# Performance work log

Measured on AMD Instinct MI355X. Metric: run time of the kernel, lower is better.

## Reference

```python
import jax, jax.numpy as jnp
import numpy as np

H, W = 352, 1216
K = 8                 # points_per_pixel (z-buffer depth)
RADIUS_PX = 1.5       # splat radius in pixels
RAD_POW = 2.0         # opts.rad_pow
TAU = 1.0             # opts.tau


def _rasterize(pts):
    # pts: [B,P,3] with xy in NDC [-1,1], z>0.
    # Returns idx [B,H,W,K] int32 (packed point index, -1 = empty),
    # dist2 [B,H,W,K] squared NDC distance to pixel center, and NDC radius r.
    B, P, _ = pts.shape
    r = RADIUS_PX / max(H, W) * 2.0
    hx = int(np.ceil(r * W / 2.0))   # splat half-extent in pixels (x)
    hy = int(np.ceil(r * H / 2.0))   # splat half-extent in pixels (y)
    dy, dx = np.meshgrid(np.arange(-hy, hy + 1), np.arange(-hx, hx + 1), indexing='ij')
    dy = jnp.asarray(dy.ravel()); dx = jnp.asarray(dx.ravel())     # [Wn]
    x, y, z = pts[..., 0], pts[..., 1], pts[..., 2]                # [B,P]
    i0 = jnp.floor((y + 1.0) * 0.5 * H).astype(jnp.int32)
    j0 = jnp.floor((x + 1.0) * 0.5 * W).astype(jnp.int32)
    ii = i0[..., None] + dy                                        # [B,P,Wn]
    jj = j0[..., None] + dx
    xc = (jj + 0.5) * (2.0 / W) - 1.0                              # pixel centers (NDC)
    yc = (ii + 0.5) * (2.0 / H) - 1.0
    d2 = (x[..., None] - xc) ** 2 + (y[..., None] - yc) ** 2
    valid = (ii >= 0) & (ii < H) & (jj >= 0) & (jj < W) & (d2 < r * r) & (z[..., None] > 0)
    NPIX = B * H * W
    pix = jnp.where(valid, (jnp.arange(B)[:, None, None] * H + ii) * W + jj, NPIX)
    pid = jnp.broadcast_to((jnp.arange(B)[:, None] * P + jnp.arange(P)[None, :])[..., None], pix.shape)
    pixf = pix.reshape(-1)
    zf = jnp.broadcast_to(z[..., None], pix.shape).reshape(-1)
    d2f = d2.reshape(-1)
    pidf = pid.reshape(-1)
    # sort candidates by (pixel, z): gives nearest-first z-buffer ordering per pixel
    order = jnp.lexsort((zf, pixf))
    pixs, d2s, pids = pixf[order], d2f[order], pidf[order]
    first = jnp.searchsorted(pixs, pixs, side='left')
    rank = jnp.arange(pixs.shape[0]) - first      # z-rank within each pixel
    keep = (rank < K) & (pixs < NPIX)
    tp = jnp.where(keep, pixs, NPIX)              # sentinel row NPIX collects rejects
    tr = jnp.where(keep, rank, 0)
    idx = jnp.full((NPIX + 1, K), -1, jnp.int32).at[tp, tr].set(
        jnp.where(keep, pids, -1).astype(jnp.int32))
    dist2 = jnp.zeros((NPIX + 1, K), pts.dtype).at[tp, tr].set(
        jnp.where(keep, d2s, jnp.zeros((), pts.dtype)))
    return idx[:NPIX].reshape(B, H, W, K), dist2[:NPIX].reshape(B, H, W, K), r


def _forward(pts3D, src):
    B, C, P = src.shape
    idx, dist2, r = _rasterize(pts3D)
    dist = dist2 / (r ** RAD_POW)
    alphas = (1.0 - jnp.sqrt(jnp.clip(dist, 0.001, 1.0))) ** TAU   # [B,H,W,K]
    feats = src.transpose(0, 2, 1).reshape(B * P, C)               # features_packed [B*P,C]
    acc = jnp.zeros((B, H, W, C), src.dtype)
    for k in range(K):   # fixed small depth-layer loop: weighted_sum compositing
        ik = idx[..., k]
        wk = jnp.where(ik >= 0, alphas[..., k], 0.0)
        acc = acc + wk[..., None] * feats[jnp.clip(ik, 0)]
    return acc.transpose(0, 3, 1, 2)                               # [B,C,H,W]


def setup_inputs():
    key = jax.random.key(0)
    k1, k2, k3 = jax.random.split(key, 3)
    B, P, C = 2, 65536, 64
    xy = jax.random.uniform(k1, (B, P, 2), minval=-1.0, maxval=1.0)
    z = jax.random.uniform(k2, (B, P, 1), minval=0.5, maxval=20.0)
    pts3D = jnp.concatenate([xy, z], axis=-1)
    src = jax.random.normal(k3, (B, C, P), dtype=jnp.float32)
    return {"pts3D": pts3D, "src": src}


def reference(pts3D, src):
    return _forward(pts3D, src)
```

## Files before the change

kernel.cpp:

```cpp
#include <hip/hip_runtime.h>
#include <cstdint>
#include <cstddef>

#define HH 352
#define WW 1216
#define KK 8
#define PP 65536
#define BB 2
#define CC 64

#define RD (1.5 / 1216.0 * 2.0)


static __device__ __forceinline__ unsigned int bf16pack_rn(float a, float b) {
    unsigned int ua = __float_as_uint(a), ub = __float_as_uint(b);
    ua = (ua + 0x7FFFu + ((ua >> 16) & 1u)) >> 16;
    ub = (ub + 0x7FFFu + ((ub >> 16) & 1u)) >> 16;
    return (ub << 16) | ua;
}

static __device__ __forceinline__ void scatter_body(const float* __restrict__ pts,
                                                    unsigned int* __restrict__ slots,
                                                    int tid) {
    const int b = tid >> 16;
    const float x = pts[tid * 3 + 0];
    const float y = pts[tid * 3 + 1];
    const float z = pts[tid * 3 + 2];
    if (!(z > 0.f)) return;

    const int i0 = (int)floorf((y + 1.f) * 0.5f * (float)HH);
    if (i0 < 0 || i0 >= HH) return;
    const int j0 = (int)floorf((x + 1.f) * 0.5f * (float)WW);

    const float yc = ((float)i0 + 0.5f) * (2.f / (float)HH) - 1.f;
    const float dyv = y - yc;
    const float dy2 = dyv * dyv;
    const float r2 = (float)(RD * RD);

    unsigned int fb = __float_as_uint(z) >> 13;
    fb = fb < 0x1F800u ? 0x1F800u : fb;
    fb = fb > 0x217FFu ? 0x217FFu : fb;
    const unsigned int key = ((fb - 0x1F800u) << 17) | (unsigned int)tid;

    const unsigned int rowbase = (unsigned int)(b * HH + i0) * WW;

    #pragma unroll
    for (int dx = -1; dx <= 1; ++dx) {
        const int jj = j0 + dx;
        if (jj < 0 || jj >= WW) continue;
        const float xc = ((float)jj + 0.5f) * (2.f / (float)WW) - 1.f;
        const float dxv = x - xc;
        if (!(dxv * dxv + dy2 < r2)) continue;

        unsigned int* s = slots + (size_t)(rowbase + jj) * KK;
        unsigned int cur = key;
        #pragma unroll
        for (int k = 0; k < KK; ++k) {
            unsigned int old = atomicMin(&s[k], cur);
            if (old & 0x80000000u) break;
            cur = old > cur ? old : cur;
        }
    }
}

#define TRANS_BLOCKS (BB * (PP / 64))
#define SCATTER_BLOCKS ((BB * PP) / 256)

__global__ __launch_bounds__(256) void prep_kernel(const float* __restrict__ pts,
                                                   const float* __restrict__ src,
                                                   unsigned int* __restrict__ slots,
                                                   unsigned int* __restrict__ feats) {
    __shared__ float tile[64][65];
    if (blockIdx.x < TRANS_BLOCKS) {
        const int bid = blockIdx.x;
        const int b = bid >> 10;
        const int p0 = (bid & 1023) * 64;
        const float* sb = src + (size_t)b * CC * PP;
        #pragma unroll
        for (int i = 0; i < 16; ++i) {
            const int idx = threadIdx.x + i * 256;
            const int c = idx >> 6;
            const int p = idx & 63;
            tile[p][c] = sb[(size_t)c * PP + (p0 + p)];
        }
        __syncthreads();
        unsigned int* fbp = feats + ((size_t)b * PP + p0) * (CC / 2);
        #pragma unroll
        for (int i = 0; i < 8; ++i) {
            const int idx = threadIdx.x + i * 256;
            const int p = idx >> 5;
            const int cp = idx & 31;
            fbp[(size_t)p * (CC / 2) + cp] = bf16pack_rn(tile[p][2 * cp], tile[p][2 * cp + 1]);
        }
        return;
    }
    scatter_body(pts, slots, (blockIdx.x - TRANS_BLOCKS) * 256 + threadIdx.x);
}

__global__ __launch_bounds__(256) void scatter_kernel(const float* __restrict__ pts,
                                                      unsigned int* __restrict__ slots) {
    scatter_body(pts, slots, blockIdx.x * 256 + threadIdx.x);
}

__global__ __launch_bounds__(256) void composite_kernel(const float* __restrict__ pts,
                                                        const unsigned int* __restrict__ feats,
                                                        const unsigned int* __restrict__ slots,
                                                        float* __restrict__ out) {
    const int HWp = HH * WW;
    const int pix = blockIdx.x * 64 + (threadIdx.x & 63);
    const int cg  = threadIdx.x >> 6;
    const int b  = pix / HWp;
    const int hw = pix - b * HWp;
    const int h = hw / WW;
    const int w = hw - h * WW;

    const uint4* sv = (const uint4*)(slots + (size_t)pix * KK);
    const uint4 sa = sv[0], sb4 = sv[1];
    const unsigned int keys[KK] = {sa.x, sa.y, sa.z, sa.w, sb4.x, sb4.y, sb4.z, sb4.w};

    const float xc = ((float)w + 0.5f) * (2.f / (float)WW) - 1.f;
    const float yc = ((float)h + 0.5f) * (2.f / (float)HH) - 1.f;
    const float invr2 = (float)(1.0 / (RD * RD));

    float acc[16];
    #pragma unroll
    for (int c = 0; c < 16; ++c) acc[c] = 0.f;

    #pragma unroll
    for (int k = 0; k < KK; ++k) {
        const unsigned int key = keys[k];
        if (key & 0x80000000u) break;
        const int pid = (int)(key & 0x1FFFFu);
        const float px = pts[pid * 3 + 0];
        const float py = pts[pid * 3 + 1];
        const float ddx = px - xc;
        const float ddy = py - yc;
        float dist = (ddx * ddx + ddy * ddy) * invr2;
        dist = fminf(fmaxf(dist, 0.001f), 1.0f);
        const float a = 1.f - sqrtf(dist);

        const uint4* f = (const uint4*)(feats + (size_t)pid * (CC / 2) + cg * 8);
        #pragma unroll
        for (int j = 0; j < 2; ++j) {
            const uint4 q = f[j];
            acc[8 * j + 0] += a * __uint_as_float(q.x << 16);
            acc[8 * j + 1] += a * __uint_as_float(q.x & 0xFFFF0000u);
            acc[8 * j + 2] += a * __uint_as_float(q.y << 16);
            acc[8 * j + 3] += a * __uint_as_float(q.y & 0xFFFF0000u);
            acc[8 * j + 4] += a * __uint_as_float(q.z << 16);
            acc[8 * j + 5] += a * __uint_as_float(q.z & 0xFFFF0000u);
            acc[8 * j + 6] += a * __uint_as_float(q.w << 16);
            acc[8 * j + 7] += a * __uint_as_float(q.w & 0xFFFF0000u);
        }
    }

    float* ob = out + (size_t)b * CC * HWp + (size_t)(cg * 16) * HWp + hw;
    #pragma unroll
    for (int c = 0; c < 16; ++c)
        __builtin_nontemporal_store(acc[c], ob + (size_t)c * HWp);
}

__global__ __launch_bounds__(256) void composite_direct(const float* __restrict__ pts,
                                                        const float* __restrict__ src,
                                                        const unsigned int* __restrict__ slots,
                                                        float* __restrict__ out) {
    const int HWp = HH * WW;
    const int tid = blockIdx.x * blockDim.x + threadIdx.x;
    const int b = tid / HWp;
    const int hw = tid - b * HWp;
    const int h = hw / WW;
    const int w = hw - h * WW;

    const uint4* sv = (const uint4*)(slots + (size_t)tid * KK);
    const uint4 sa = sv[0], sb4 = sv[1];
    const unsigned int keys[KK] = {sa.x, sa.y, sa.z, sa.w, sb4.x, sb4.y, sb4.z, sb4.w};

    const float xc = ((float)w + 0.5f) * (2.f / (float)WW) - 1.f;
    const float yc = ((float)h + 0.5f) * (2.f / (float)HH) - 1.f;
    const float invr2 = (float)(1.0 / (RD * RD));

    float alpha[KK];
    int   pidx[KK];
    int n = 0;
    #pragma unroll
    for (int k = 0; k < KK; ++k) {
        const unsigned int key = keys[k];
        if (key & 0x80000000u) break;
        const int pid = (int)(key & 0x1FFFFu);
        const float px = pts[pid * 3 + 0];
        const float py = pts[pid * 3 + 1];
        const float ddx = px - xc;
        const float ddy = py - yc;
        float dist = (ddx * ddx + ddy * ddy) * invr2;
        dist = fminf(fmaxf(dist, 0.001f), 1.0f);
        alpha[k] = 1.f - sqrtf(dist);
        pidx[k]  = pid & (PP - 1);
        n = k + 1;
    }

    const float* sbp = src + (size_t)b * CC * PP;
    float* ob = out + (size_t)b * CC * HWp + hw;
    for (int c = 0; c < CC; ++c) {
        float acc = 0.f;
        #pragma unroll
        for (int k = 0; k < KK; ++k)
            if (k < n) acc += alpha[k] * sbp[(size_t)c * PP + pidx[k]];
        __builtin_nontemporal_store(acc, ob + (size_t)c * HWp);
    }
}

extern "C" void kernel_launch(void* const* d_in, const int* in_sizes, int n_in,
                              void* d_out, int out_size, void* d_ws, size_t ws_size,
                              hipStream_t stream) {
    const float* pts = (const float*)d_in[0];
    const float* src = (const float*)d_in[1];
    float* out = (float*)d_out;

    const size_t slot_bytes  = (size_t)BB * HH * WW * KK * sizeof(unsigned int);
    const size_t feats_bytes = (size_t)BB * PP * CC * 2;
    const size_t need = slot_bytes + feats_bytes;

    if (ws_size >= need + 256) {
        char* base = (char*)d_ws + ((ws_size - need) & ~(size_t)255);
        unsigned int* feats = (unsigned int*)base;
        unsigned int* slots = (unsigned int*)(base + feats_bytes);

        prep_kernel<<<TRANS_BLOCKS + SCATTER_BLOCKS, 256, 0, stream>>>(pts, src, slots, feats);
        const int comp_blocks = (BB * HH * WW) / 64;
        composite_kernel<<<comp_blocks, 256, 0, stream>>>(pts, feats, slots, out);
    } else {
        unsigned int* slots = (unsigned int*)d_ws;
        scatter_kernel<<<SCATTER_BLOCKS, 256, 0, stream>>>(pts, slots);
        composite_direct<<<(BB * HH * WW) / 256, 256, 0, stream>>>(pts, src, slots, out);
    }
}
```

Baseline: 259.2 us.

## Remap composite threads to 4 pixels x 4 channels with vectorized stores

Reorganizes the composite kernel so each thread handles four consecutive pixels and four channels, instead of one pixel and sixteen channels. Each block now covers 256 pixels for one of four 16-channel groups. Output writes become 16-byte vector nontemporal stores along the pixel dimension, replacing scalar strided stores. The cost is redundant slot and point reads across the four channel blocks, and smaller 8-byte feature loads per key.

```diff
diff --git a/kernel.cpp b/kernel.cpp
--- a/kernel.cpp
+++ b/kernel.cpp
@@ -11,6 +11,8 @@
 
 #define RD (1.5 / 1216.0 * 2.0)
 
+
+typedef float vf4 __attribute__((ext_vector_type(4)));
 
 static __device__ __forceinline__ unsigned int bf16pack_rn(float a, float b) {
     unsigned int ua = __float_as_uint(a), ub = __float_as_uint(b);
@@ -102,30 +104,12 @@
     scatter_body(pts, slots, blockIdx.x * 256 + threadIdx.x);
 }
 
-__global__ __launch_bounds__(256) void composite_kernel(const float* __restrict__ pts,
-                                                        const unsigned int* __restrict__ feats,
-                                                        const unsigned int* __restrict__ slots,
-                                                        float* __restrict__ out) {
-    const int HWp = HH * WW;
-    const int pix = blockIdx.x * 64 + (threadIdx.x & 63);
-    const int cg  = threadIdx.x >> 6;
-    const int b  = pix / HWp;
-    const int hw = pix - b * HWp;
-    const int h = hw / WW;
-    const int w = hw - h * WW;
-
-    const uint4* sv = (const uint4*)(slots + (size_t)pix * KK);
-    const uint4 sa = sv[0], sb4 = sv[1];
-    const unsigned int keys[KK] = {sa.x, sa.y, sa.z, sa.w, sb4.x, sb4.y, sb4.z, sb4.w};
-
-    const float xc = ((float)w + 0.5f) * (2.f / (float)WW) - 1.f;
-    const float yc = ((float)h + 0.5f) * (2.f / (float)HH) - 1.f;
-    const float invr2 = (float)(1.0 / (RD * RD));
-
-    float acc[16];
-    #pragma unroll
-    for (int c = 0; c < 16; ++c) acc[c] = 0.f;
-
+static __device__ __forceinline__ void do_pixel(const float* __restrict__ pts,
+                                                const unsigned int* __restrict__ feats,
+                                                uint4 ka, uint4 kb,
+                                                float xc, float yc, int ch0,
+                                                float invr2, float acc[4]) {
+    const unsigned int keys[KK] = {ka.x, ka.y, ka.z, ka.w, kb.x, kb.y, kb.z, kb.w};
     #pragma unroll
     for (int k = 0; k < KK; ++k) {
         const unsigned int key = keys[k];
@@ -138,26 +122,61 @@
         float dist = (ddx * ddx + ddy * ddy) * invr2;
         dist = fminf(fmaxf(dist, 0.001f), 1.0f);
         const float a = 1.f - sqrtf(dist);
-
-        const uint4* f = (const uint4*)(feats + (size_t)pid * (CC / 2) + cg * 8);
-        #pragma unroll
-        for (int j = 0; j < 2; ++j) {
-            const uint4 q = f[j];
-            acc[8 * j + 0] += a * __uint_as_float(q.x << 16);
-            acc[8 * j + 1] += a * __uint_as_float(q.x & 0xFFFF0000u);
-            acc[8 * j + 2] += a * __uint_as_float(q.y << 16);
-            acc[8 * j + 3] += a * __uint_as_float(q.y & 0xFFFF0000u);
-            acc[8 * j + 4] += a * __uint_as_float(q.z << 16);
-            acc[8 * j + 5] += a * __uint_as_float(q.z & 0xFFFF0000u);
-            acc[8 * j + 6] += a * __uint_as_float(q.w << 16);
-            acc[8 * j + 7] += a * __uint_as_float(q.w & 0xFFFF0000u);
-        }
-    }
-
-    float* ob = out + (size_t)b * CC * HWp + (size_t)(cg * 16) * HWp + hw;
-    #pragma unroll
-    for (int c = 0; c < 16; ++c)
-        __builtin_nontemporal_store(acc[c], ob + (size_t)c * HWp);
+        const uint2 q = *(const uint2*)(feats + (size_t)pid * (CC / 2) + (ch0 >> 1));
+        acc[0] += a * __uint_as_float(q.x << 16);
+        acc[1] += a * __uint_as_float(q.x & 0xFFFF0000u);
+        acc[2] += a * __uint_as_float(q.y << 16);
+        acc[3] += a * __uint_as_float(q.y & 0xFFFF0000u);
+    }
+}
+
+__global__ __launch_bounds__(256) void composite_kernel(const float* __restrict__ pts,
+                                                        const unsigned int* __restrict__ feats,
+                                                        const unsigned int* __restrict__ slots,
+                                                        float* __restrict__ out) {
+    const int HWp = HH * WW;
+    const int lane = threadIdx.x & 63;
+    const int wv   = threadIdx.x >> 6;
+    const int pxblk = blockIdx.x >> 2;
+    const int cb    = blockIdx.x & 3;
+    const int px0 = pxblk * 256 + lane * 4;
+    const int ch0 = cb * 16 + wv * 4;
+
+    const int b   = px0 / HWp;
+    const int hw0 = px0 - b * HWp;
+
+    const uint4* sv = (const uint4*)(slots + (size_t)px0 * KK);
+    const uint4 s0 = sv[0], s1 = sv[1], s2 = sv[2], s3 = sv[3];
+    const uint4 s4 = sv[4], s5 = sv[5], s6 = sv[6], s7 = sv[7];
+
+    const float invr2 = (float)(1.0 / (RD * RD));
+    float acc[4][4];
+    #pragma unroll
+    for (int i = 0; i < 4; ++i)
+        #pragma unroll
+        for (int j = 0; j < 4; ++j) acc[i][j] = 0.f;
+
+    #pragma unroll
+    for (int i = 0; i < 4; ++i) {
+        const int hw = hw0 + i;
+        const int h = hw / WW;
+        const int w = hw - h * WW;
+        const float xc = ((float)w + 0.5f) * (2.f / (float)WW) - 1.f;
+        const float yc = ((float)h + 0.5f) * (2.f / (float)HH) - 1.f;
+        switch (i) {
+            case 0: do_pixel(pts, feats, s0, s1, xc, yc, ch0, invr2, acc[0]); break;
+            case 1: do_pixel(pts, feats, s2, s3, xc, yc, ch0, invr2, acc[1]); break;
+            case 2: do_pixel(pts, feats, s4, s5, xc, yc, ch0, invr2, acc[2]); break;
+            case 3: do_pixel(pts, feats, s6, s7, xc, yc, ch0, invr2, acc[3]); break;
+        }
+    }
+
+    float* ob = out + ((size_t)b * CC + ch0) * HWp + hw0;
+    #pragma unroll
+    for (int j = 0; j < 4; ++j) {
+        vf4 v = {acc[0][j], acc[1][j], acc[2][j], acc[3][j]};
+        __builtin_nontemporal_store(v, (vf4*)(ob + (size_t)j * HWp));
+    }
 }
 
 __global__ __launch_bounds__(256) void composite_direct(const float* __restrict__ pts,
```

New measurement: 310.8 us. 1.2x slower.
